# Performance work log

Measured on AMD Instinct MI355X. Metric: run time of the kernel, lower is better.

Reference implementation:

```python
import jax, jax.numpy as jnp
import numpy as np

B, L, D = 4, 896, 2048
HQ, HKV, HD = 32, 8, 64
GROUP = HQ // HKV          # 4
TOKENS_PER_FRAME = 7
ROPE_BASE = 10000.0


def setup_inputs() -> dict:
    key = jax.random.key(0)
    ks = jax.random.split(key, 5)
    s = 0.02
    return {
        "x": jax.random.normal(ks[0], (B, L, D), jnp.float32),
        "wq": jax.random.normal(ks[1], (D, D), jnp.float32) * s,
        "wk": jax.random.normal(ks[2], (D, HKV * HD), jnp.float32) * s,
        "wv": jax.random.normal(ks[3], (D, HKV * HD), jnp.float32) * s,
        "wo": jax.random.normal(ks[4], (D, D), jnp.float32) * s,
        "pos_ids": jnp.arange(L, dtype=jnp.int32),
    }


def _apply_rotary(t, cos, sin):
    # t: [B, L, H, HD]; rotate all HD dims, interleaved pairs.
    Bt, Lt, Ht, Hd = t.shape
    tp = t.reshape(Bt, Lt, Ht, Hd // 2, 2)
    x1, x2 = tp[..., 0], tp[..., 1]
    c = cos[None, :, None, :]   # [1, L, 1, HD/2]
    s = sin[None, :, None, :]
    y1 = x1 * c - x2 * s
    y2 = x1 * s + x2 * c
    return jnp.stack([y1, y2], axis=-1).reshape(Bt, Lt, Ht, Hd)


def reference(x, wq, wk, wv, wo, pos_ids):
    Bx, Lx, Dx = x.shape
    q = (x @ wq).reshape(Bx, Lx, HQ, HD)
    k = (x @ wk).reshape(Bx, Lx, HKV, HD)
    v = (x @ wv).reshape(Bx, Lx, HKV, HD)

    # RoPE (rot_dim = head_dim), scale = 1.0
    half = HD // 2
    inv_freq = 1.0 / (ROPE_BASE ** (jnp.arange(half, dtype=jnp.float32) / half))
    freqs = pos_ids.astype(jnp.float32)[:, None] * inv_freq[None, :]  # [L, HD/2]
    cos, sin = jnp.cos(freqs), jnp.sin(freqs)
    q = _apply_rotary(q, cos, sin)
    k = _apply_rotary(k, cos, sin)

    # GQA: expand kv heads to q heads (kv_head = q_head // GROUP)
    k = jnp.repeat(k, GROUP, axis=2)   # [B, L, HQ, HD]
    v = jnp.repeat(v, GROUP, axis=2)

    scale = 1.0 / jnp.sqrt(jnp.float32(HD))
    scores = jnp.einsum('blhd,bmhd->bhlm', q, k) * scale  # [B, HQ, L, L]

    # frame-block causal mask: allow key frame <= query frame
    pos = jnp.arange(Lx)
    fid = pos // TOKENS_PER_FRAME
    allow = fid[None, :] <= fid[:, None]                  # [L, L]
    neg = jnp.finfo(scores.dtype).min
    scores = jnp.where(allow[None, None], scores, neg)

    probs = jax.nn.softmax(scores, axis=-1)
    out = jnp.einsum('bhlm,bmhd->blhd', probs, v).reshape(Bx, Lx, Dx)
    return out @ wo
```

## Files before the change

### kernel.cpp

```cpp
#include <hip/hip_runtime.h>
#include <hip/hip_bf16.h>
#include <cstdint>

typedef __bf16 bf16;
typedef __bf16 bf16x8 __attribute__((ext_vector_type(8)));
typedef float floatx4 __attribute__((ext_vector_type(4)));

#define B_   4
#define L_   896
#define D_   2048
#define HQ_  32
#define HKV_ 8
#define HD_  64
#define NQKV 3072
#define M_   3584

__device__ inline void gl_lds16(const bf16* g, bf16* l) {
    __builtin_amdgcn_global_load_lds(
        (const __attribute__((address_space(1))) void*)g,
        (__attribute__((address_space(3))) void*)l, 16, 0, 0);
}

__device__ inline void barrier_() {
    asm volatile("" ::: "memory");
    __builtin_amdgcn_s_barrier();
    asm volatile("" ::: "memory");
}

__global__ __launch_bounds__(256) void convert_to_bf16(const float* __restrict__ in,
                                                       bf16* __restrict__ out) {
    long q = (long)blockIdx.x * 256 + threadIdx.x;
    float4 v = ((const float4*)in)[q];
    union { bf16 b[4]; ushort4 u; } w;
    w.b[0] = (bf16)v.x; w.b[1] = (bf16)v.y; w.b[2] = (bf16)v.z; w.b[3] = (bf16)v.w;
    ((ushort4*)out)[q] = w.u;
}

__global__ __launch_bounds__(256) void rope_cs_kernel(const int* __restrict__ pos_ids,
                                                      float2* __restrict__ cs) {
    int idx = blockIdx.x * 256 + threadIdx.x;
    if (idx >= L_ * 32) return;
    int l = idx >> 5, i = idx & 31;
    float p = (float)pos_ids[l];
    float inv = exp2f(-(float)i * (13.287712379549449f / 32.0f));
    float a = p * inv;
    cs[idx] = make_float2(cosf(a), sinf(a));
}

__global__ __launch_bounds__(256) void rope_apply(bf16* __restrict__ QKV,
                                                  const float2* __restrict__ cs) {
    int idx = blockIdx.x * 256 + threadIdx.x;
    int m = idx / 320, g = idx - m * 320;
    int l = m % L_;
    int hp = (g * 4) & 31;
    const float2* ct = &cs[l * 32 + hp];
    bf16* p = QKV + (long)m * NQKV + g * 8;
    bf16x8 v = *(bf16x8*)p;
    bf16x8 w;
#pragma unroll
    for (int i = 0; i < 4; i++) {
        float2 csv = ct[i];
        float x1 = (float)v[2 * i], x2 = (float)v[2 * i + 1];
        w[2 * i]     = (bf16)(x1 * csv.x - x2 * csv.y);
        w[2 * i + 1] = (bf16)(x1 * csv.y + x2 * csv.x);
    }
    *(bf16x8*)p = w;
}

__global__ __launch_bounds__(256) void transpose_cvt(
    const float* __restrict__ in, ushort* __restrict__ out, int C, int R) {
    __shared__ ushort t[64][72];
    int tid = threadIdx.x;
    int tr = tid >> 4, tc = (tid & 15) << 2;
    long r0 = (long)blockIdx.y << 6, c0 = (long)blockIdx.x << 6;
#pragma unroll
    for (int i = 0; i < 4; ++i) {
        float4 v = *(const float4*)&in[(r0 + tr + i * 16) * C + c0 + tc];
        union { bf16 b[4]; ushort4 u; } w;
        w.b[0] = (bf16)v.x; w.b[1] = (bf16)v.y; w.b[2] = (bf16)v.z; w.b[3] = (bf16)v.w;
        *(ushort4*)&t[tr + i * 16][tc] = w.u;
    }
    __syncthreads();
#pragma unroll
    for (int i = 0; i < 4; ++i) {
        ushort4 w;
        w.x = t[tc + 0][tr + i * 16];
        w.y = t[tc + 1][tr + i * 16];
        w.z = t[tc + 2][tr + i * 16];
        w.w = t[tc + 3][tr + i * 16];
        *(ushort4*)&out[(c0 + tr + i * 16) * R + r0 + tc] = w;
    }
}

__global__ __launch_bounds__(256) void transpose_u16(
    const ushort* __restrict__ in, ushort* __restrict__ out,
    int ld_in, int ld_out, long is1, long is2, long os1, long os2) {
    __shared__ ushort t[64][72];
    int z = blockIdx.z;
    const ushort* ip = in + (long)(z >> 3) * is1 + (long)(z & 7) * is2;
    ushort* op = out + (long)(z >> 3) * os1 + (long)(z & 7) * os2;
    int tid = threadIdx.x;
    int tr = tid >> 4, tc = (tid & 15) << 2;
    long r0 = (long)blockIdx.y << 6, c0 = (long)blockIdx.x << 6;
#pragma unroll
    for (int i = 0; i < 4; ++i) {
        ushort4 v = *(const ushort4*)&ip[(r0 + tr + i * 16) * ld_in + c0 + tc];
        *(ushort4*)&t[tr + i * 16][tc] = v;
    }
    __syncthreads();
#pragma unroll
    for (int i = 0; i < 4; ++i) {
        ushort4 w;
        w.x = t[tc + 0][tr + i * 16];
        w.y = t[tc + 1][tr + i * 16];
        w.z = t[tc + 2][tr + i * 16];
        w.w = t[tc + 3][tr + i * 16];
        *(ushort4*)&op[(c0 + tr + i * 16) * ld_out + r0 + tc] = w;
    }
}


template <int RQ>
__device__ inline void lda(const bf16* p, int l16, int c0, int c1, bf16x8 (&af)[4][2]) {
#pragma unroll
    for (int i = 0; i < 4; ++i) {
        const bf16* rp = &p[(RQ * 64 + i * 16 + l16) * 64];
        af[i][0] = *(const bf16x8*)&rp[c0];
        af[i][1] = *(const bf16x8*)&rp[c1];
    }
}

template <int CQ>
__device__ inline void ldb(const bf16* p, int brow, int l16, int c0, int c1,
                           bf16x8 (&bq)[2][2]) {
#pragma unroll
    for (int j = 0; j < 2; ++j) {
        const bf16* rp = &p[(brow + (CQ * 2 + j) * 16 + l16) * 64];
        bq[j][0] = *(const bf16x8*)&rp[c0];
        bq[j][1] = *(const bf16x8*)&rp[c1];
    }
}

template <int RQ, int CQ>
__device__ inline void mma(const bf16x8 (&af)[4][2], const bf16x8 (&bq)[2][2],
                           floatx4 (&acc)[8][4]) {
#pragma unroll
    for (int i = 0; i < 4; ++i)
#pragma unroll
        for (int j = 0; j < 2; ++j) {
            floatx4 c = acc[RQ * 4 + i][CQ * 2 + j];
            c = __builtin_amdgcn_mfma_f32_16x16x32_bf16(af[i][0], bq[j][0], c, 0, 0, 0);
            c = __builtin_amdgcn_mfma_f32_16x16x32_bf16(af[i][1], bq[j][1], c, 0, 0, 0);
            acc[RQ * 4 + i][CQ * 2 + j] = c;
        }
}

__device__ inline void stage_half(const bf16* gsrc, bf16* ldst, long rowK) {
    gl_lds16(gsrc,            ldst);
    gl_lds16(gsrc + 8 * rowK, ldst + 512);
}

__global__ __launch_bounds__(512, 2) void gemm256(
    const bf16* __restrict__ A, const bf16* __restrict__ Bt, void* __restrict__ C,
    int Ntot, int Ktot, int outf32) {
    __shared__ bf16 lds[2][2][2][128 * 64];
    const int tid = threadIdx.x;
    const int w = tid >> 6, lane = tid & 63;
    const int quad = lane >> 4, l16 = lane & 15;
    const int wr = w >> 2, wc = w & 3;

    const int gx = gridDim.x;
    const int nwg = gx * gridDim.y;
    int orig = blockIdx.y * gx + blockIdx.x;
    int q8 = nwg >> 3, r8 = nwg & 7;
    int xcd = orig & 7, lid = orig >> 3;
    int wg = (xcd < r8 ? xcd * (q8 + 1) : r8 * (q8 + 1) + (xcd - r8) * q8) + lid;
    const long m0 = (long)(wg / gx) << 8;
    const long n0 = (long)(wg % gx) << 8;

    const long rowK = Ktot;
    const int srow = w * 16 + (lane >> 3);
    const int scol = ((lane & 7) ^ (lane >> 3)) << 3;
    const bf16* baseA = A  + (m0 + srow) * rowK + scol;
    const bf16* baseB = Bt + (n0 + srow) * rowK + scol;
    const int d0 = w * 1024 + lane * 8;

    const int m7 = l16 & 7;
    const int col0 = ((0 + quad) ^ m7) << 3;
    const int col1 = ((4 + quad) ^ m7) << 3;
    const int brow = (wc & 1) * 64;

    floatx4 acc[8][4];
#pragma unroll
    for (int i = 0; i < 8; ++i)
#pragma unroll
        for (int j = 0; j < 4; ++j)
#pragma unroll
            for (int r = 0; r < 4; ++r) acc[i][j][r] = 0.f;

    bf16x8 af[4][2], bq0[2][2], bq1[2][2];

    const int T = Ktot >> 6;
    stage_half(baseA,                   &lds[0][0][0][d0], rowK);
    stage_half(baseA + 128 * rowK,      &lds[0][0][1][d0], rowK);
    stage_half(baseB,                   &lds[0][1][0][d0], rowK);
    stage_half(baseB + 128 * rowK,      &lds[0][1][1][d0], rowK);
    stage_half(baseB + 64,              &lds[1][1][0][d0], rowK);
    stage_half(baseB + 128 * rowK + 64, &lds[1][1][1][d0], rowK);
    asm volatile("s_waitcnt vmcnt(4)" ::: "memory");
    barrier_();

    for (int t = 0; t < T; ++t) {
        const int cur = t & 1, nxt = cur ^ 1;
        const bf16* pa = &lds[cur][0][wr][0];
        const bf16* pb = &lds[cur][1][wc >> 1][0];
        const long koff  = (long)(t + 1) * 64;
        const long koff2 = (long)(t + 2) * 64;

        lda<0>(pa, l16, col0, col1, af);
        ldb<0>(pb, brow, l16, col0, col1, bq0);
        if (t + 1 < T) stage_half(baseA + koff, &lds[nxt][0][0][d0], rowK);
        barrier_();
        asm volatile("s_waitcnt lgkmcnt(0)" ::: "memory");
        __builtin_amdgcn_sched_barrier(0);
        __builtin_amdgcn_s_setprio(1);
        mma<0, 0>(af, bq0, acc);
        __builtin_amdgcn_s_setprio(0);
        barrier_();

        ldb<1>(pb, brow, l16, col0, col1, bq1);
        if (t + 1 < T) stage_half(baseA + 128 * rowK + koff, &lds[nxt][0][1][d0], rowK);
        barrier_();
        asm volatile("s_waitcnt lgkmcnt(0)" ::: "memory");
        __builtin_amdgcn_sched_barrier(0);
        __builtin_amdgcn_s_setprio(1);
        mma<0, 1>(af, bq1, acc);
        __builtin_amdgcn_s_setprio(0);
        barrier_();

        lda<1>(pa, l16, col0, col1, af);
        if (t + 2 < T) stage_half(baseB + koff2, &lds[cur][1][0][d0], rowK);
        barrier_();
        asm volatile("s_waitcnt lgkmcnt(0)" ::: "memory");
        __builtin_amdgcn_sched_barrier(0);
        __builtin_amdgcn_s_setprio(1);
        mma<1, 0>(af, bq0, acc);
        __builtin_amdgcn_s_setprio(0);
        barrier_();

        if (t + 2 < T) stage_half(baseB + 128 * rowK + koff2, &lds[cur][1][1][d0], rowK);
        barrier_();
        asm volatile("s_waitcnt lgkmcnt(0)" ::: "memory");
        __builtin_amdgcn_sched_barrier(0);
        __builtin_amdgcn_s_setprio(1);
        mma<1, 1>(af, bq1, acc);
        __builtin_amdgcn_s_setprio(0);
        if (t + 2 < T) asm volatile("s_waitcnt vmcnt(4)" ::: "memory");
        else           asm volatile("s_waitcnt vmcnt(0)" ::: "memory");
        barrier_();
    }

#pragma unroll
    for (int ri = 0; ri < 8; ++ri)
#pragma unroll
        for (int j = 0; j < 4; ++j)
#pragma unroll
            for (int r = 0; r < 4; ++r) {
                long m = m0 + wr * 128 + ri * 16 + quad * 4 + r;
                long n = n0 + wc * 64 + j * 16 + l16;
                if (outf32) ((float*)C)[m * Ntot + n] = acc[ri][j][r];
                else        ((bf16*)C)[m * Ntot + n] = (bf16)acc[ri][j][r];
            }
}

__global__ __launch_bounds__(256) void attn_kernel(
    const bf16* __restrict__ QKV,
    const bf16* __restrict__ Vt,
    bf16* __restrict__ AO) {
    __shared__ bf16 Ks[64 * 72];
    __shared__ bf16 Vs[64 * 72];
    __shared__ bf16 Ps[4][16 * 72];
    const int tid  = threadIdx.x;
    const int wid  = tid >> 6, lane = tid & 63;
    const int quad = lane >> 4, c = lane & 15;
    const int b = blockIdx.z, hq = blockIdx.y, kvh = hq >> 2;
    const int q0b = blockIdx.x * 64;
    const int q0 = q0b + wid * 16;
    bf16* ps = &Ps[wid][0];

    const bf16* Qb = QKV + ((long)(b * L_ + q0)) * NQKV + hq * HD_;
    const bf16* Kb = QKV + ((long)(b * L_)) * NQKV + D_ + kvh * HD_;
    const bf16* Vb = Vt + ((long)(b * HKV_ + kvh)) * (HD_ * L_);

    bf16x8 qf0 = *(const bf16x8*)&Qb[(long)c * NQKV + quad * 8];
    bf16x8 qf1 = *(const bf16x8*)&Qb[(long)c * NQKV + 32 + quad * 8];

    float lsum[4];
    floatx4 o[4];
#pragma unroll
    for (int r = 0; r < 4; r++) lsum[r] = 0.f;
#pragma unroll
    for (int nt = 0; nt < 4; nt++)
#pragma unroll
        for (int r = 0; r < 4; r++) o[nt][r] = 0.f;

    int fe[4];
#pragma unroll
    for (int r = 0; r < 4; r++) { int l = q0 + quad * 4 + r; fe[r] = (l / 7 + 1) * 7; }
    const int kend = ((q0b + 63) / 7 + 1) * 7;

    const int srow = tid >> 3, schunk = (tid & 7) << 3;

    for (int k0 = 0; k0 < kend; k0 += 64) {
        bf16x8 kg0 = *(const bf16x8*)&Kb[(long)(k0 + srow) * NQKV + schunk];
        bf16x8 kg1 = *(const bf16x8*)&Kb[(long)(k0 + 32 + srow) * NQKV + schunk];
        bf16x8 vg0 = *(const bf16x8*)&Vb[(long)srow * L_ + k0 + schunk];
        bf16x8 vg1 = *(const bf16x8*)&Vb[(long)(srow + 32) * L_ + k0 + schunk];
        __syncthreads();
        *(bf16x8*)&Ks[srow * 72 + schunk]        = kg0;
        *(bf16x8*)&Ks[(srow + 32) * 72 + schunk] = kg1;
        *(bf16x8*)&Vs[srow * 72 + schunk]        = vg0;
        *(bf16x8*)&Vs[(srow + 32) * 72 + schunk] = vg1;
        __syncthreads();

        floatx4 s[4];
#pragma unroll
        for (int n = 0; n < 4; n++) {
#pragma unroll
            for (int r = 0; r < 4; r++) s[n][r] = 0.f;
            bf16x8 kf0 = *(bf16x8*)&Ks[(n * 16 + c) * 72 + quad * 8];
            bf16x8 kf1 = *(bf16x8*)&Ks[(n * 16 + c) * 72 + 32 + quad * 8];
            s[n] = __builtin_amdgcn_mfma_f32_16x16x32_bf16(qf0, kf0, s[n], 0, 0, 0);
            s[n] = __builtin_amdgcn_mfma_f32_16x16x32_bf16(qf1, kf1, s[n], 0, 0, 0);
        }
#pragma unroll
        for (int n = 0; n < 4; n++) {
            const int key = k0 + n * 16 + c;
#pragma unroll
            for (int r = 0; r < 4; r++) {
                float e = __expf(fmaf(s[n][r], 0.125f, -12.0f));
                e = (key < fe[r]) ? e : 0.f;
                lsum[r] += e;
                ps[(quad * 4 + r) * 72 + n * 16 + c] = (bf16)e;
            }
        }
        bf16x8 pf0 = *(bf16x8*)&ps[c * 72 + quad * 8];
        bf16x8 pf1 = *(bf16x8*)&ps[c * 72 + 32 + quad * 8];
#pragma unroll
        for (int nt = 0; nt < 4; nt++) {
            bf16x8 vf0 = *(bf16x8*)&Vs[(nt * 16 + c) * 72 + quad * 8];
            bf16x8 vf1 = *(bf16x8*)&Vs[(nt * 16 + c) * 72 + 32 + quad * 8];
            o[nt] = __builtin_amdgcn_mfma_f32_16x16x32_bf16(pf0, vf0, o[nt], 0, 0, 0);
            o[nt] = __builtin_amdgcn_mfma_f32_16x16x32_bf16(pf1, vf1, o[nt], 0, 0, 0);
        }
    }
#pragma unroll
    for (int r = 0; r < 4; r++) {
#pragma unroll
        for (int off = 1; off < 16; off <<= 1) lsum[r] += __shfl_xor(lsum[r], off);
    }
#pragma unroll
    for (int nt = 0; nt < 4; nt++)
#pragma unroll
        for (int r = 0; r < 4; r++) {
            int l = q0 + quad * 4 + r;
            AO[((long)(b * L_ + l)) * D_ + hq * HD_ + nt * 16 + c] = (bf16)(o[nt][r] / lsum[r]);
        }
}

extern "C" void kernel_launch(void* const* d_in, const int* in_sizes, int n_in,
                              void* d_out, int out_size, void* d_ws, size_t ws_size,
                              hipStream_t stream) {
    (void)in_sizes; (void)n_in; (void)out_size; (void)ws_size;
    const float* x  = (const float*)d_in[0];
    const float* wq = (const float*)d_in[1];
    const float* wk = (const float*)d_in[2];
    const float* wv = (const float*)d_in[3];
    const float* wo = (const float*)d_in[4];
    const int* pos  = (const int*)d_in[5];

    bf16* ws    = (bf16*)d_ws;
    bf16* xb    = ws;
    bf16* wqkvT = ws + 7340032L;
    bf16* woT   = ws + 13631488L;
    bf16* QKV   = ws + 17825792L;
    bf16* Vt    = ws + 28835840L;
    bf16* AO    = xb;
    float2* cs  = (float2*)(ws + 30670848L);

    convert_to_bf16<<<dim3(7168), 256, 0, stream>>>(x, xb);
    rope_cs_kernel<<<dim3(112), dim3(256), 0, stream>>>(pos, cs);

    transpose_cvt<<<dim3(32, 32), 256, 0, stream>>>(wq, (ushort*)wqkvT, 2048, 2048);
    transpose_cvt<<<dim3(8, 32), 256, 0, stream>>>(wk, (ushort*)(wqkvT + 4194304L), 512, 2048);
    transpose_cvt<<<dim3(8, 32), 256, 0, stream>>>(wv, (ushort*)(wqkvT + 5242880L), 512, 2048);
    transpose_cvt<<<dim3(32, 32), 256, 0, stream>>>(wo, (ushort*)woT, 2048, 2048);

    gemm256<<<dim3(12, 14), 512, 0, stream>>>(xb, wqkvT, QKV, NQKV, D_, 0);

    rope_apply<<<dim3(4480), 256, 0, stream>>>(QKV, cs);

    transpose_u16<<<dim3(1, 14, 32), 256, 0, stream>>>(
        (const ushort*)(QKV + 2560), (ushort*)Vt, 3072, 896,
        896L * 3072, 64, 8L * 57344, 57344);

    attn_kernel<<<dim3(14, 32, 4), 256, 0, stream>>>(QKV, Vt, AO);

    gemm256<<<dim3(8, 14), 512, 0, stream>>>(AO, woT, d_out, D_, D_, 1);
}
```

Before: 302.3 us.

## Fuse RoPE into QKV GEMM epilogue and use 256x128 tiles for output projection

Removes the separate rope_apply pass by applying the rotary rotation in the QKV GEMM epilogue, with a lane-pair shuffle supplying the partner element. This saves a full read and write of the Q/K part of QKV. It also adds a 256x128-tile GEMM with a triple-buffered B stage for the output projection, which raises the workgroup count from 112 to 224 so more of the 256 CUs are busy. The cost is extra cos/sin loads in the epilogue and a new, less-tested GEMM schedule.

```diff
diff --git a/kernel.cpp b/kernel.cpp
--- a/kernel.cpp
+++ b/kernel.cpp
@@ -45,26 +45,6 @@
     float inv = exp2f(-(float)i * (13.287712379549449f / 32.0f));
     float a = p * inv;
     cs[idx] = make_float2(cosf(a), sinf(a));
-}
-
-__global__ __launch_bounds__(256) void rope_apply(bf16* __restrict__ QKV,
-                                                  const float2* __restrict__ cs) {
-    int idx = blockIdx.x * 256 + threadIdx.x;
-    int m = idx / 320, g = idx - m * 320;
-    int l = m % L_;
-    int hp = (g * 4) & 31;
-    const float2* ct = &cs[l * 32 + hp];
-    bf16* p = QKV + (long)m * NQKV + g * 8;
-    bf16x8 v = *(bf16x8*)p;
-    bf16x8 w;
-#pragma unroll
-    for (int i = 0; i < 4; i++) {
-        float2 csv = ct[i];
-        float x1 = (float)v[2 * i], x2 = (float)v[2 * i + 1];
-        w[2 * i]     = (bf16)(x1 * csv.x - x2 * csv.y);
-        w[2 * i + 1] = (bf16)(x1 * csv.y + x2 * csv.x);
-    }
-    *(bf16x8*)p = w;
 }
 
 __global__ __launch_bounds__(256) void transpose_cvt(
@@ -120,19 +100,19 @@
 }
 
 
-template <int RQ>
-__device__ inline void lda(const bf16* p, int l16, int c0, int c1, bf16x8 (&af)[4][2]) {
+template <int RQ, int RESPAN>
+__device__ inline void lda_g(const bf16* p, int l16, int c0, int c1, bf16x8 (&af)[4][2]) {
 #pragma unroll
     for (int i = 0; i < 4; ++i) {
-        const bf16* rp = &p[(RQ * 64 + i * 16 + l16) * 64];
+        const bf16* rp = &p[(RQ * RESPAN + i * 16 + l16) * 64];
         af[i][0] = *(const bf16x8*)&rp[c0];
         af[i][1] = *(const bf16x8*)&rp[c1];
     }
 }
 
 template <int CQ>
-__device__ inline void ldb(const bf16* p, int brow, int l16, int c0, int c1,
-                           bf16x8 (&bq)[2][2]) {
+__device__ inline void ldb_g(const bf16* p, int brow, int l16, int c0, int c1,
+                             bf16x8 (&bq)[2][2]) {
 #pragma unroll
     for (int j = 0; j < 2; ++j) {
         const bf16* rp = &p[(brow + (CQ * 2 + j) * 16 + l16) * 64];
@@ -141,9 +121,14 @@
     }
 }
 
+__device__ inline void stage_half(const bf16* gsrc, bf16* ldst, long rowK) {
+    gl_lds16(gsrc,            ldst);
+    gl_lds16(gsrc + 8 * rowK, ldst + 512);
+}
+
 template <int RQ, int CQ>
-__device__ inline void mma(const bf16x8 (&af)[4][2], const bf16x8 (&bq)[2][2],
-                           floatx4 (&acc)[8][4]) {
+__device__ inline void mma8(const bf16x8 (&af)[4][2], const bf16x8 (&bq)[2][2],
+                            floatx4 (&acc)[8][4]) {
 #pragma unroll
     for (int i = 0; i < 4; ++i)
 #pragma unroll
@@ -155,14 +140,9 @@
         }
 }
 
-__device__ inline void stage_half(const bf16* gsrc, bf16* ldst, long rowK) {
-    gl_lds16(gsrc,            ldst);
-    gl_lds16(gsrc + 8 * rowK, ldst + 512);
-}
-
 __global__ __launch_bounds__(512, 2) void gemm256(
     const bf16* __restrict__ A, const bf16* __restrict__ Bt, void* __restrict__ C,
-    int Ntot, int Ktot, int outf32) {
+    int Ntot, int Ktot, int outf32, int ropeflag, const float2* __restrict__ cs) {
     __shared__ bf16 lds[2][2][2][128 * 64];
     const int tid = threadIdx.x;
     const int w = tid >> 6, lane = tid & 63;
@@ -217,34 +197,34 @@
         const long koff  = (long)(t + 1) * 64;
         const long koff2 = (long)(t + 2) * 64;
 
-        lda<0>(pa, l16, col0, col1, af);
-        ldb<0>(pb, brow, l16, col0, col1, bq0);
+        lda_g<0, 64>(pa, l16, col0, col1, af);
+        ldb_g<0>(pb, brow, l16, col0, col1, bq0);
         if (t + 1 < T) stage_half(baseA + koff, &lds[nxt][0][0][d0], rowK);
         barrier_();
         asm volatile("s_waitcnt lgkmcnt(0)" ::: "memory");
         __builtin_amdgcn_sched_barrier(0);
         __builtin_amdgcn_s_setprio(1);
-        mma<0, 0>(af, bq0, acc);
+        mma8<0, 0>(af, bq0, acc);
         __builtin_amdgcn_s_setprio(0);
         barrier_();
 
-        ldb<1>(pb, brow, l16, col0, col1, bq1);
+        ldb_g<1>(pb, brow, l16, col0, col1, bq1);
         if (t + 1 < T) stage_half(baseA + 128 * rowK + koff, &lds[nxt][0][1][d0], rowK);
         barrier_();
         asm volatile("s_waitcnt lgkmcnt(0)" ::: "memory");
         __builtin_amdgcn_sched_barrier(0);
         __builtin_amdgcn_s_setprio(1);
-        mma<0, 1>(af, bq1, acc);
+        mma8<0, 1>(af, bq1, acc);
         __builtin_amdgcn_s_setprio(0);
         barrier_();
 
-        lda<1>(pa, l16, col0, col1, af);
+        lda_g<1, 64>(pa, l16, col0, col1, af);
         if (t + 2 < T) stage_half(baseB + koff2, &lds[cur][1][0][d0], rowK);
         barrier_();
         asm volatile("s_waitcnt lgkmcnt(0)" ::: "memory");
         __builtin_amdgcn_sched_barrier(0);
         __builtin_amdgcn_s_setprio(1);
-        mma<1, 0>(af, bq0, acc);
+        mma8<1, 0>(af, bq0, acc);
         __builtin_amdgcn_s_setprio(0);
         barrier_();
 
@@ -253,13 +233,15 @@
         asm volatile("s_waitcnt lgkmcnt(0)" ::: "memory");
         __builtin_amdgcn_sched_barrier(0);
         __builtin_amdgcn_s_setprio(1);
-        mma<1, 1>(af, bq1, acc);
+        mma8<1, 1>(af, bq1, acc);
         __builtin_amdgcn_s_setprio(0);
         if (t + 2 < T) asm volatile("s_waitcnt vmcnt(4)" ::: "memory");
         else           asm volatile("s_waitcnt vmcnt(0)" ::: "memory");
         barrier_();
     }
 
+    const int dorope = ropeflag && (n0 < 2560);
+    const float sgn = (lane & 1) ? 1.f : -1.f;
 #pragma unroll
     for (int ri = 0; ri < 8; ++ri)
 #pragma unroll
@@ -268,8 +250,128 @@
             for (int r = 0; r < 4; ++r) {
                 long m = m0 + wr * 128 + ri * 16 + quad * 4 + r;
                 long n = n0 + wc * 64 + j * 16 + l16;
-                if (outf32) ((float*)C)[m * Ntot + n] = acc[ri][j][r];
-                else        ((bf16*)C)[m * Ntot + n] = (bf16)acc[ri][j][r];
+                float v = acc[ri][j][r];
+                if (dorope) {
+                    int l = (int)(m % L_);
+                    float2 csv = cs[l * 32 + ((int)(n >> 1) & 31)];
+                    float p = __shfl_xor(v, 1);
+                    v = v * csv.x + p * sgn * csv.y;
+                }
+                if (outf32) ((float*)C)[m * Ntot + n] = v;
+                else        ((bf16*)C)[m * Ntot + n] = (bf16)v;
+            }
+}
+
+template <int CH>
+__device__ inline void mma4(const bf16x8 (&af)[4][2], const bf16x8 (&bq)[2][2],
+                            floatx4 (&acc)[4][4]) {
+#pragma unroll
+    for (int i = 0; i < 4; ++i)
+#pragma unroll
+        for (int j = 0; j < 2; ++j) {
+            floatx4 c = acc[i][CH * 2 + j];
+            c = __builtin_amdgcn_mfma_f32_16x16x32_bf16(af[i][0], bq[j][0], c, 0, 0, 0);
+            c = __builtin_amdgcn_mfma_f32_16x16x32_bf16(af[i][1], bq[j][1], c, 0, 0, 0);
+            acc[i][CH * 2 + j] = c;
+        }
+}
+
+__global__ __launch_bounds__(512, 2) void gemm256x128(
+    const bf16* __restrict__ A, const bf16* __restrict__ Bt, float* __restrict__ C,
+    int Ntot, int Ktot) {
+    __shared__ bf16 ldsA[2][2][128 * 64];
+    __shared__ bf16 ldsB[3][128 * 64];
+    const int tid = threadIdx.x;
+    const int w = tid >> 6, lane = tid & 63;
+    const int quad = lane >> 4, l16 = lane & 15;
+    const int wr = w >> 1, wc = w & 1;
+
+    const int gx = gridDim.x;
+    const int nwg = gx * gridDim.y;
+    int orig = blockIdx.y * gx + blockIdx.x;
+    int q8 = nwg >> 3, r8 = nwg & 7;
+    int xcd = orig & 7, lid = orig >> 3;
+    int wg = (xcd < r8 ? xcd * (q8 + 1) : r8 * (q8 + 1) + (xcd - r8) * q8) + lid;
+    const long m0 = (long)(wg / gx) << 8;
+    const long n0 = (long)(wg % gx) << 7;
+
+    const long rowK = Ktot;
+    const int srow = w * 16 + (lane >> 3);
+    const int scol = ((lane & 7) ^ (lane >> 3)) << 3;
+    const bf16* baseA = A  + (m0 + srow) * rowK + scol;
+    const bf16* baseB = Bt + (n0 + srow) * rowK + scol;
+    const int d0 = w * 1024 + lane * 8;
+
+    const int m7 = l16 & 7;
+    const int col0 = ((0 + quad) ^ m7) << 3;
+    const int col1 = ((4 + quad) ^ m7) << 3;
+    const int arow = (wr & 1) * 64;
+    const int brow = wc * 64;
+
+    floatx4 acc[4][4];
+#pragma unroll
+    for (int i = 0; i < 4; ++i)
+#pragma unroll
+        for (int j = 0; j < 4; ++j)
+#pragma unroll
+            for (int r = 0; r < 4; ++r) acc[i][j][r] = 0.f;
+
+    bf16x8 af[4][2], bq0[2][2], bq1[2][2];
+
+    const int T = Ktot >> 6;
+    stage_half(baseA,              &ldsA[0][0][d0], rowK);
+    stage_half(baseA + 128 * rowK, &ldsA[0][1][d0], rowK);
+    stage_half(baseB,              &ldsB[0][d0],    rowK);
+    stage_half(baseB + 64,         &ldsB[1][d0],    rowK);
+    asm volatile("s_waitcnt vmcnt(2)" ::: "memory");
+    barrier_();
+
+    int bs = 0;
+    for (int t = 0; t < T; ++t) {
+        const int cur = t & 1, nxt = cur ^ 1;
+        const bf16* pa = &ldsA[cur][wr >> 1][0];
+        const bf16* pb = &ldsB[bs][0];
+        const long koff  = (long)(t + 1) * 64;
+        const long koff2 = (long)(t + 2) * 64;
+        const int bs2 = bs >= 1 ? bs - 1 : 2;
+
+        lda_g<0, 0>(pa, arow + l16, col0, col1, af);
+        ldb_g<0>(pb, brow, l16, col0, col1, bq0);
+        if (t + 1 < T) {
+            stage_half(baseA + koff,              &ldsA[nxt][0][d0], rowK);
+            stage_half(baseA + 128 * rowK + koff, &ldsA[nxt][1][d0], rowK);
+        }
+        barrier_();
+        asm volatile("s_waitcnt lgkmcnt(0)" ::: "memory");
+        __builtin_amdgcn_sched_barrier(0);
+        __builtin_amdgcn_s_setprio(1);
+        mma4<0>(af, bq0, acc);
+        __builtin_amdgcn_s_setprio(0);
+        barrier_();
+
+        ldb_g<1>(pb, brow, l16, col0, col1, bq1);
+        if (t + 2 < T) stage_half(baseB + koff2, &ldsB[bs2][d0], rowK);
+        barrier_();
+        asm volatile("s_waitcnt lgkmcnt(0)" ::: "memory");
+        __builtin_amdgcn_sched_barrier(0);
+        __builtin_amdgcn_s_setprio(1);
+        mma4<1>(af, bq1, acc);
+        __builtin_amdgcn_s_setprio(0);
+        if      (t + 2 < T) asm volatile("s_waitcnt vmcnt(2)" ::: "memory");
+        else if (t + 1 < T) asm volatile("s_waitcnt vmcnt(0)" ::: "memory");
+        barrier_();
+        bs = bs < 2 ? bs + 1 : 0;
+    }
+
+#pragma unroll
+    for (int i = 0; i < 4; ++i)
+#pragma unroll
+        for (int j = 0; j < 4; ++j)
+#pragma unroll
+            for (int r = 0; r < 4; ++r) {
+                long m = m0 + wr * 64 + i * 16 + quad * 4 + r;
+                long n = n0 + wc * 64 + j * 16 + l16;
+                C[m * Ntot + n] = acc[i][j][r];
             }
 }
 
@@ -396,9 +498,7 @@
     transpose_cvt<<<dim3(8, 32), 256, 0, stream>>>(wv, (ushort*)(wqkvT + 5242880L), 512, 2048);
     transpose_cvt<<<dim3(32, 32), 256, 0, stream>>>(wo, (ushort*)woT, 2048, 2048);
 
-    gemm256<<<dim3(12, 14), 512, 0, stream>>>(xb, wqkvT, QKV, NQKV, D_, 0);
-
-    rope_apply<<<dim3(4480), 256, 0, stream>>>(QKV, cs);
+    gemm256<<<dim3(12, 14), 512, 0, stream>>>(xb, wqkvT, QKV, NQKV, D_, 0, 1, cs);
 
     transpose_u16<<<dim3(1, 14, 32), 256, 0, stream>>>(
         (const ushort*)(QKV + 2560), (ushort*)Vt, 3072, 896,
@@ -406,5 +506,5 @@
 
     attn_kernel<<<dim3(14, 32, 4), 256, 0, stream>>>(QKV, Vt, AO);
 
-    gemm256<<<dim3(8, 14), 512, 0, stream>>>(AO, woT, d_out, D_, D_, 1);
-}
+    gemm256x128<<<dim3(16, 14), 512, 0, stream>>>(AO, woT, (float*)d_out, D_, D_);
+}
```

Result: no change. 306.9 us (+1.5%).
